# Optimization experiments

Measured on AMD Instinct MI355X. Metric: run time of the kernel, lower is better.

The kernel has to match this reference:

```python
import jax, jax.numpy as jnp
import numpy as np

N_HEAD = 16
N_KV_HEAD = 4
D_MODEL = 2048
D_HEAD = 128
D_OUT = 2048
N_REP = N_HEAD // N_KV_HEAD
Q_INNER = N_HEAD * D_HEAD
KV_INNER = N_KV_HEAD * D_HEAD
B, S = 2, 2048


def setup_inputs() -> dict:
    key = jax.random.key(0)
    ks = jax.random.split(key, 10)
    sc = lambda fan_in: 1.0 / np.sqrt(fan_in)
    return {
        "hidden_state": jax.random.normal(ks[0], (B, S, D_MODEL), dtype=jnp.float32),
        "attention_mask": jnp.ones((B, 1, S, S), dtype=jnp.int32),
        "Wq": jax.random.uniform(ks[1], (Q_INNER, D_MODEL), jnp.float32, -sc(D_MODEL), sc(D_MODEL)),
        "bq": jax.random.uniform(ks[2], (Q_INNER,), jnp.float32, -sc(D_MODEL), sc(D_MODEL)),
        "Wk": jax.random.uniform(ks[3], (KV_INNER, D_MODEL), jnp.float32, -sc(D_MODEL), sc(D_MODEL)),
        "bk": jax.random.uniform(ks[4], (KV_INNER,), jnp.float32, -sc(D_MODEL), sc(D_MODEL)),
        "Wv": jax.random.uniform(ks[5], (KV_INNER, D_MODEL), jnp.float32, -sc(D_MODEL), sc(D_MODEL)),
        "bv": jax.random.uniform(ks[6], (KV_INNER,), jnp.float32, -sc(D_MODEL), sc(D_MODEL)),
        "Wo": jax.random.uniform(ks[7], (D_OUT, Q_INNER), jnp.float32, -sc(Q_INNER), sc(Q_INNER)),
        "bo": jax.random.uniform(ks[8], (D_OUT,), jnp.float32, -sc(Q_INNER), sc(Q_INNER)),
    }


def reference(hidden_state, attention_mask, Wq, bq, Wk, bk, Wv, bv, Wo, bo):
    b, s, _ = hidden_state.shape
    # projections (torch Linear: x @ W.T + b)
    q = hidden_state @ Wq.T + bq                    # [b, s, n_head*d_head]
    k = hidden_state @ Wk.T + bk                    # [b, s, n_kv*d_head]
    v = hidden_state @ Wv.T + bv
    q = q.reshape(b, s, N_HEAD, D_HEAD).transpose(0, 2, 1, 3)      # [b, h, s, d]
    k = k.reshape(b, s, N_KV_HEAD, D_HEAD).transpose(0, 2, 1, 3)   # [b, kh, s, d]
    v = v.reshape(b, s, N_KV_HEAD, D_HEAD).transpose(0, 2, 1, 3)
    # repeat_kv: expand kv heads to n_head
    k = jnp.repeat(k, N_REP, axis=1)                # [b, h, s, d]
    v = jnp.repeat(v, N_REP, axis=1)
    scores = jnp.einsum("bhqd,bhkd->bhqk", q, k) / jnp.sqrt(jnp.float32(D_HEAD))
    scores = jnp.where(attention_mask == 0, -jnp.inf, scores)
    probs = jax.nn.softmax(scores, axis=-1)         # [b, h, s, s]
    out = jnp.einsum("bhqk,bhkd->bhqd", probs, v)   # [b, h, s, d]
    out = out.transpose(0, 2, 1, 3).reshape(b, s, Q_INNER)
    return out @ Wo.T + bo                          # [b, s, d_out]
```

## Files before the change

### kernel.cpp

```cpp
#include <hip/hip_runtime.h>

typedef unsigned short u16;
typedef unsigned int u32;
typedef __attribute__((ext_vector_type(4))) float f32x4;
typedef __attribute__((ext_vector_type(16))) float f32x16;
typedef __attribute__((ext_vector_type(2))) u32 u32x2;
typedef __attribute__((ext_vector_type(4))) u32 u32x4;
typedef __attribute__((ext_vector_type(8))) __bf16 bf16x8;

#define QSCALE (0.08838834764831845f * 1.44269504088896340736f)

__device__ __forceinline__ u16 f2bf(float x) {
  u32 u = __builtin_bit_cast(u32, x);
  u32 r = (u + 0x7FFFu + ((u >> 16) & 1u)) >> 16;
  return (u16)r;
}

__device__ __forceinline__ u16 cvt_bf16(float x) {
  __bf16 b = (__bf16)x;
  return __builtin_bit_cast(u16, b);
}

__device__ __forceinline__ u32 pk2(float lo, float hi) {
  return (u32)cvt_bf16(lo) | ((u32)cvt_bf16(hi) << 16);
}

__device__ __forceinline__ f32x16 mfma32(bf16x8 a, bf16x8 b, f32x16 c) {
  return __builtin_amdgcn_mfma_f32_32x32x16_bf16(a, b, c, 0, 0, 0);
}

#define GLDS16(g, l)                                              \
  __builtin_amdgcn_global_load_lds(                               \
      (const __attribute__((address_space(1))) void*)(g),         \
      (__attribute__((address_space(3))) void*)(l), 16, 0, 0)

__global__ __launch_bounds__(256) void cvt_kernel(const float* __restrict__ src,
                                                  u16* __restrict__ dst) {
  size_t i = (size_t)blockIdx.x * 256 + threadIdx.x;
  float4 a = ((const float4*)src)[2 * i];
  float4 b = ((const float4*)src)[2 * i + 1];
  uint4 r;
  r.x = f2bf(a.x) | ((u32)f2bf(a.y) << 16);
  r.y = f2bf(a.z) | ((u32)f2bf(a.w) << 16);
  r.z = f2bf(b.x) | ((u32)f2bf(b.y) << 16);
  r.w = f2bf(b.z) | ((u32)f2bf(b.w) << 16);
  ((uint4*)dst)[i] = r;
}

__device__ __forceinline__ void gemm_bt_core(const u16* __restrict__ A,
                                             const u16* __restrict__ B, int K,
                                             int bm, int bn, u16* As, u16* Bs,
                                             f32x4 acc[4][4]) {
  const int tid = threadIdx.x;
  const int lane = tid & 63;
  const int w = tid >> 6;
  const int wm = (w >> 1) * 64;
  const int wn = (w & 1) * 64;
  const int r0 = lane & 15;
  const int g = lane >> 4;
  const int c = w * 64 + lane;
  const int arow = c >> 2;
  const int acol = (c & 3) * 8;

  for (int k0 = 0; k0 < K; k0 += 32) {
    GLDS16(A + (size_t)(bm + arow) * K + k0 + acol, As + w * 512);
    GLDS16(A + (size_t)(bm + 64 + arow) * K + k0 + acol, As + 2048 + w * 512);
    GLDS16(B + (size_t)(bn + arow) * K + k0 + acol, Bs + w * 512);
    GLDS16(B + (size_t)(bn + 64 + arow) * K + k0 + acol, Bs + 2048 + w * 512);
    __syncthreads();
    bf16x8 af[4], bf[4];
#pragma unroll
    for (int mi = 0; mi < 4; ++mi)
      af[mi] = *(const bf16x8*)&As[(wm + mi * 16 + r0) * 32 + g * 8];
#pragma unroll
    for (int ni = 0; ni < 4; ++ni)
      bf[ni] = *(const bf16x8*)&Bs[(wn + ni * 16 + r0) * 32 + g * 8];
#pragma unroll
    for (int mi = 0; mi < 4; ++mi)
#pragma unroll
      for (int ni = 0; ni < 4; ++ni)
        acc[mi][ni] = __builtin_amdgcn_mfma_f32_16x16x32_bf16(af[mi], bf[ni],
                                                              acc[mi][ni], 0, 0, 0);
    __syncthreads();
  }
}

__global__ __launch_bounds__(256, 2) void qkv_gemm(
    const u16* __restrict__ A, const u16* __restrict__ B,
    const float* __restrict__ bq, const float* __restrict__ bk,
    const float* __restrict__ bv, u16* __restrict__ qb, u16* __restrict__ kb,
    u16* __restrict__ vtb) {
  __shared__ u16 As[4096], Bs[4096];
  f32x4 acc[4][4];
#pragma unroll
  for (int i = 0; i < 4; ++i)
#pragma unroll
    for (int j = 0; j < 4; ++j) acc[i][j] = f32x4{0.f, 0.f, 0.f, 0.f};
  const int bm = blockIdx.y * 128, bn = blockIdx.x * 128;
  gemm_bt_core(A, B, 2048, bm, bn, As, Bs, acc);
  const int lane = threadIdx.x & 63, w = threadIdx.x >> 6;
  const int wm = (w >> 1) * 64, wn = (w & 1) * 64;
  const int r0 = lane & 15, g = lane >> 4;
#pragma unroll
  for (int ni = 0; ni < 4; ++ni) {
    const int n = bn + wn + ni * 16 + r0;
#pragma unroll
    for (int mi = 0; mi < 4; ++mi) {
      f32x4 v = acc[mi][ni];
#pragma unroll
      for (int r = 0; r < 4; ++r) {
        const int m = bm + wm + mi * 16 + g * 4 + r;
        const int b = m >> 11, s = m & 2047;
        const float val = v[r];
        if (n < 2048) {
          const int h = n >> 7, d = n & 127;
          qb[((size_t)(b * 16 + h) * 2048 + s) * 128 + d] =
              f2bf((val + bq[n]) * QSCALE);
        } else if (n < 2560) {
          const int nn = n - 2048, kh = nn >> 7, d = nn & 127;
          kb[((size_t)(b * 4 + kh) * 2048 + s) * 128 + d] = f2bf(val + bk[nn]);
        } else {
          const int nn = n - 2560, kh = nn >> 7, d = nn & 127;
          vtb[((size_t)(b * 4 + kh) * 128 + d) * 2048 + s] = f2bf(val + bv[nn]);
        }
      }
    }
  }
}

__global__ __launch_bounds__(256, 2) void oproj_gemm(const u16* __restrict__ A,
                                                     const u16* __restrict__ B,
                                                     const float* __restrict__ bo,
                                                     float* __restrict__ out) {
  __shared__ u16 As[4096], Bs[4096];
  f32x4 acc[4][4];
#pragma unroll
  for (int i = 0; i < 4; ++i)
#pragma unroll
    for (int j = 0; j < 4; ++j) acc[i][j] = f32x4{0.f, 0.f, 0.f, 0.f};
  const int bm = blockIdx.y * 128, bn = blockIdx.x * 128;
  gemm_bt_core(A, B, 2048, bm, bn, As, Bs, acc);
  const int lane = threadIdx.x & 63, w = threadIdx.x >> 6;
  const int wm = (w >> 1) * 64, wn = (w & 1) * 64;
  const int r0 = lane & 15, g = lane >> 4;
#pragma unroll
  for (int ni = 0; ni < 4; ++ni) {
    const int n = bn + wn + ni * 16 + r0;
    const float bb = bo[n];
#pragma unroll
    for (int mi = 0; mi < 4; ++mi) {
#pragma unroll
      for (int r = 0; r < 4; ++r) {
        const int m = bm + wm + mi * 16 + g * 4 + r;
        out[(size_t)m * 2048 + n] = acc[mi][ni][r] + bb;
      }
    }
  }
}

__global__ __launch_bounds__(256, 2) void attn_kernel(const u16* __restrict__ q,
                                                      const u16* __restrict__ k,
                                                      const u16* __restrict__ vt,
                                                      u16* __restrict__ o) {
  __shared__ u16 Ks[2][8192];
  __shared__ u16 Vs[2][8192];
  const int tid = threadIdx.x, lane = tid & 63, w = tid >> 6;
  const int l31 = lane & 31, hi = lane >> 5;
  const int b = blockIdx.z, h = blockIdx.y, kh = h >> 2;
  const int q0 = blockIdx.x * 128 + w * 32;
  const u16* qh = q + ((size_t)(b * 16 + h) * 2048 + q0) * 128;
  const u16* kp = k + (size_t)(b * 4 + kh) * 2048 * 128;
  const u16* vp = vt + (size_t)(b * 4 + kh) * 128 * 2048;

  bf16x8 qa[8];
#pragma unroll
  for (int dc = 0; dc < 8; ++dc)
    qa[dc] = *(const bf16x8*)&qh[(size_t)l31 * 128 + dc * 16 + hi * 8];

  f32x16 oacc[4];
#pragma unroll
  for (int dt = 0; dt < 4; ++dt) oacc[dt] = (f32x16)(0.f);
  float mrun = -INFINITY, lrun = 0.f;

  const int gB = w * 64 + lane;

#define STAGE_KV(cur, t)                                                       \
  do {                                                                         \
    const u16* kt_ = kp + (size_t)(t) * 64 * 128;                              \
    _Pragma("unroll") for (int i_ = 0; i_ < 4; ++i_) {                         \
      int gi_ = i_ * 256 + gB;                                                 \
      int row_ = gi_ >> 4, gc_ = gi_ & 15;                                     \
      GLDS16(kt_ + row_ * 128 + ((gc_ ^ (row_ & 15)) * 8),                     \
             &Ks[cur][(i_ * 256 + w * 64) * 8]);                               \
    }                                                                          \
    _Pragma("unroll") for (int i_ = 0; i_ < 4; ++i_) {                         \
      int gi_ = i_ * 256 + gB;                                                 \
      int row_ = gi_ >> 3, gc_ = gi_ & 7;                                      \
      GLDS16(vp + (size_t)row_ * 2048 + (t) * 64 + ((gc_ ^ (row_ & 7)) * 8),   \
             &Vs[cur][(i_ * 256 + w * 64) * 8]);                               \
    }                                                                          \
  } while (0)

  STAGE_KV(0, 0);
  __syncthreads();
  int cur = 0;

  for (int t = 0; t < 32; ++t) {
    if (t < 31) STAGE_KV(cur ^ 1, t + 1);

    f32x16 s0v = (f32x16)(0.f), s1v = (f32x16)(0.f);
    __builtin_amdgcn_s_setprio(1);
#pragma unroll
    for (int dc = 0; dc < 8; ++dc) {
      const int gc = dc * 2 + hi;
      const int ro0 = l31, ro1 = 32 + l31;
      bf16x8 kf0 = *(const bf16x8*)&Ks[cur][ro0 * 128 + ((gc ^ (ro0 & 15)) << 3)];
      bf16x8 kf1 = *(const bf16x8*)&Ks[cur][ro1 * 128 + ((gc ^ (ro1 & 15)) << 3)];
      s0v = mfma32(kf0, qa[dc], s0v);
      s1v = mfma32(kf1, qa[dc], s1v);
    }
    __builtin_amdgcn_s_setprio(0);

    float m8[8];
#pragma unroll
    for (int i = 0; i < 8; ++i)
      m8[i] = fmaxf(fmaxf(s0v[i], s0v[i + 8]), fmaxf(s1v[i], s1v[i + 8]));
    float mx = fmaxf(fmaxf(fmaxf(m8[0], m8[1]), fmaxf(m8[2], m8[3])),
                     fmaxf(fmaxf(m8[4], m8[5]), fmaxf(m8[6], m8[7])));
    mx = fmaxf(mx, __shfl_xor(mx, 32));
    if (__any(mx > mrun + 8.f)) {
      const float mnew = fmaxf(mrun, mx);
      const float alpha = __builtin_amdgcn_exp2f(mrun - mnew);
      mrun = mnew;
      lrun *= alpha;
#pragma unroll
      for (int r = 0; r < 16; ++r) {
        const float ar = __shfl(alpha, ((r & 3) + 8 * (r >> 2)) + (hi << 2));
#pragma unroll
        for (int dt = 0; dt < 4; ++dt) oacc[dt][r] *= ar;
      }
    }
    float rsf = 0.f;
#pragma unroll
    for (int i = 0; i < 16; ++i) {
      s0v[i] = __builtin_amdgcn_exp2f(s0v[i] - mrun);
      s1v[i] = __builtin_amdgcn_exp2f(s1v[i] - mrun);
      rsf += s0v[i] + s1v[i];
    }
    lrun += rsf + __shfl_xor(rsf, 32);

    __builtin_amdgcn_s_setprio(1);
#pragma unroll
    for (int c = 0; c < 4; ++c) {
      const float* sv = (c < 2) ? (const float*)&s0v : (const float*)&s1v;
      const int base = (c & 1) * 8;
      u32x4 fw;
      fw[0] = pk2(sv[base + 0], sv[base + 1]);
      fw[1] = pk2(sv[base + 2], sv[base + 3]);
      fw[2] = pk2(sv[base + 4], sv[base + 5]);
      fw[3] = pk2(sv[base + 6], sv[base + 7]);
      const bf16x8 pf = __builtin_bit_cast(bf16x8, fw);
#pragma unroll
      for (int dt = 0; dt < 4; ++dt) {
        const int d = dt * 32 + l31;
        const u32x2 vlo =
            *(const u32x2*)&Vs[cur][d * 64 + (((2 * c) ^ (d & 7)) << 3) + 4 * hi];
        const u32x2 vhi =
            *(const u32x2*)&Vs[cur][d * 64 + (((2 * c + 1) ^ (d & 7)) << 3) + 4 * hi];
        u32x4 vv;
        vv[0] = vlo[0]; vv[1] = vlo[1]; vv[2] = vhi[0]; vv[3] = vhi[1];
        oacc[dt] = mfma32(pf, __builtin_bit_cast(bf16x8, vv), oacc[dt]);
      }
    }
    __builtin_amdgcn_s_setprio(0);

    __syncthreads();
    cur ^= 1;
  }
#undef STAGE_KV

  const float invl = 1.f / lrun;
#pragma unroll
  for (int r = 0; r < 16; ++r) {
    const int rb = (r & 3) + 8 * (r >> 2);
    const float linv = __shfl(invl, rb + (hi << 2));
    const int row = q0 + rb + (hi << 2);
#pragma unroll
    for (int dt = 0; dt < 4; ++dt)
      o[(size_t)(b * 2048 + row) * 2048 + h * 128 + dt * 32 + l31] =
          cvt_bf16(oacc[dt][r] * linv);
  }
}

extern "C" void kernel_launch(void* const* d_in, const int* in_sizes, int n_in,
                              void* d_out, int out_size, void* d_ws,
                              size_t ws_size, hipStream_t stream) {
  (void)in_sizes; (void)n_in; (void)out_size; (void)ws_size;
  const float* hidden = (const float*)d_in[0];
  const float* Wq = (const float*)d_in[2];
  const float* bq = (const float*)d_in[3];
  const float* Wk = (const float*)d_in[4];
  const float* bk = (const float*)d_in[5];
  const float* Wv = (const float*)d_in[6];
  const float* bv = (const float*)d_in[7];
  const float* Wo = (const float*)d_in[8];
  const float* bo = (const float*)d_in[9];
  float* out = (float*)d_out;
  char* ws = (char*)d_ws;

  u16* hidb = (u16*)(ws + 0);
  u16* wcat = (u16*)(ws + 16777216);
  u16* wob  = (u16*)(ws + 29360128);
  u16* qb   = (u16*)(ws + 37748736);
  u16* kb   = (u16*)(ws + 54525952);
  u16* vtb  = (u16*)(ws + 58720256);
  u16* attb = (u16*)(ws + 62914560);

  cvt_kernel<<<4096, 256, 0, stream>>>(hidden, hidb);
  cvt_kernel<<<2048, 256, 0, stream>>>(Wq, wcat);
  cvt_kernel<<<512, 256, 0, stream>>>(Wk, wcat + (size_t)2048 * 2048);
  cvt_kernel<<<512, 256, 0, stream>>>(Wv, wcat + (size_t)2560 * 2048);
  cvt_kernel<<<2048, 256, 0, stream>>>(Wo, wob);

  qkv_gemm<<<dim3(24, 32), 256, 0, stream>>>(hidb, wcat, bq, bk, bv, qb, kb, vtb);
  attn_kernel<<<dim3(16, 16, 2), 256, 0, stream>>>(qb, kb, vtb, attb);
  oproj_gemm<<<dim3(16, 32), 256, 0, stream>>>(attb, wob, bo, out);
}
```

Before: 231.0 us.

## Merge conversion launches, widen GEMM K-tile with swizzle, compute softmax denominator via MFMA

Fuses the five fp32-to-bf16 conversion launches into one kernel that picks its source and destination by block index, removing per-launch overhead. The shared GEMM core now stages 64-wide K slices with an XOR-swizzled LDS layout. This halves the barriers per K step and avoids LDS bank conflicts, at the cost of doubling LDS per block. In attention, the row-sum of probabilities is computed by an extra MFMA against a ones vector instead of scalar adds and shuffles, trading VALU work for matrix-core work.

```diff
diff --git a/kernel.cpp b/kernel.cpp
--- a/kernel.cpp
+++ b/kernel.cpp
@@ -34,17 +34,29 @@
       (const __attribute__((address_space(1))) void*)(g),         \
       (__attribute__((address_space(3))) void*)(l), 16, 0, 0)
 
-__global__ __launch_bounds__(256) void cvt_kernel(const float* __restrict__ src,
-                                                  u16* __restrict__ dst) {
-  size_t i = (size_t)blockIdx.x * 256 + threadIdx.x;
-  float4 a = ((const float4*)src)[2 * i];
-  float4 b = ((const float4*)src)[2 * i + 1];
+__global__ __launch_bounds__(256) void cvt5_kernel(
+    const float* __restrict__ s0, const float* __restrict__ s1,
+    const float* __restrict__ s2, const float* __restrict__ s3,
+    const float* __restrict__ s4, u16* __restrict__ d0, u16* __restrict__ d1,
+    u16* __restrict__ d2, u16* __restrict__ d3, u16* __restrict__ d4) {
+  const int bid = blockIdx.x;
+  const float* s;
+  u16* d;
+  int base;
+  if (bid < 4096) { s = s0; d = d0; base = 0; }
+  else if (bid < 6144) { s = s1; d = d1; base = 4096; }
+  else if (bid < 6656) { s = s2; d = d2; base = 6144; }
+  else if (bid < 7168) { s = s3; d = d3; base = 6656; }
+  else { s = s4; d = d4; base = 7168; }
+  size_t i = (size_t)(bid - base) * 256 + threadIdx.x;
+  float4 a = ((const float4*)s)[2 * i];
+  float4 b = ((const float4*)s)[2 * i + 1];
   uint4 r;
   r.x = f2bf(a.x) | ((u32)f2bf(a.y) << 16);
   r.y = f2bf(a.z) | ((u32)f2bf(a.w) << 16);
   r.z = f2bf(b.x) | ((u32)f2bf(b.y) << 16);
   r.w = f2bf(b.z) | ((u32)f2bf(b.w) << 16);
-  ((uint4*)dst)[i] = r;
+  ((uint4*)d)[i] = r;
 }
 
 __device__ __forceinline__ void gemm_bt_core(const u16* __restrict__ A,
@@ -58,29 +70,37 @@
   const int wn = (w & 1) * 64;
   const int r0 = lane & 15;
   const int g = lane >> 4;
-  const int c = w * 64 + lane;
-  const int arow = c >> 2;
-  const int acol = (c & 3) * 8;
-
-  for (int k0 = 0; k0 < K; k0 += 32) {
-    GLDS16(A + (size_t)(bm + arow) * K + k0 + acol, As + w * 512);
-    GLDS16(A + (size_t)(bm + 64 + arow) * K + k0 + acol, As + 2048 + w * 512);
-    GLDS16(B + (size_t)(bn + arow) * K + k0 + acol, Bs + w * 512);
-    GLDS16(B + (size_t)(bn + 64 + arow) * K + k0 + acol, Bs + 2048 + w * 512);
+
+  for (int k0 = 0; k0 < K; k0 += 64) {
+#pragma unroll
+    for (int i = 0; i < 4; ++i) {
+      const int gi = i * 256 + tid;
+      const int row = gi >> 3, gc = gi & 7;
+      const int scol = (gc ^ (row & 7)) * 8;
+      GLDS16(A + (size_t)(bm + row) * K + k0 + scol, As + gi * 8);
+      GLDS16(B + (size_t)(bn + row) * K + k0 + scol, Bs + gi * 8);
+    }
     __syncthreads();
-    bf16x8 af[4], bf[4];
-#pragma unroll
-    for (int mi = 0; mi < 4; ++mi)
-      af[mi] = *(const bf16x8*)&As[(wm + mi * 16 + r0) * 32 + g * 8];
-#pragma unroll
-    for (int ni = 0; ni < 4; ++ni)
-      bf[ni] = *(const bf16x8*)&Bs[(wn + ni * 16 + r0) * 32 + g * 8];
-#pragma unroll
-    for (int mi = 0; mi < 4; ++mi)
-#pragma unroll
-      for (int ni = 0; ni < 4; ++ni)
-        acc[mi][ni] = __builtin_amdgcn_mfma_f32_16x16x32_bf16(af[mi], bf[ni],
-                                                              acc[mi][ni], 0, 0, 0);
+#pragma unroll
+    for (int kh = 0; kh < 2; ++kh) {
+      bf16x8 af[4], bf[4];
+#pragma unroll
+      for (int mi = 0; mi < 4; ++mi) {
+        const int row = wm + mi * 16 + r0;
+        af[mi] = *(const bf16x8*)&As[row * 64 + (((kh * 4 + g) ^ (row & 7)) * 8)];
+      }
+#pragma unroll
+      for (int ni = 0; ni < 4; ++ni) {
+        const int row = wn + ni * 16 + r0;
+        bf[ni] = *(const bf16x8*)&Bs[row * 64 + (((kh * 4 + g) ^ (row & 7)) * 8)];
+      }
+#pragma unroll
+      for (int mi = 0; mi < 4; ++mi)
+#pragma unroll
+        for (int ni = 0; ni < 4; ++ni)
+          acc[mi][ni] = __builtin_amdgcn_mfma_f32_16x16x32_bf16(
+              af[mi], bf[ni], acc[mi][ni], 0, 0, 0);
+    }
     __syncthreads();
   }
 }
@@ -90,7 +110,7 @@
     const float* __restrict__ bq, const float* __restrict__ bk,
     const float* __restrict__ bv, u16* __restrict__ qb, u16* __restrict__ kb,
     u16* __restrict__ vtb) {
-  __shared__ u16 As[4096], Bs[4096];
+  __shared__ u16 As[8192], Bs[8192];
   f32x4 acc[4][4];
 #pragma unroll
   for (int i = 0; i < 4; ++i)
@@ -132,7 +152,7 @@
                                                      const u16* __restrict__ B,
                                                      const float* __restrict__ bo,
                                                      float* __restrict__ out) {
-  __shared__ u16 As[4096], Bs[4096];
+  __shared__ u16 As[8192], Bs[8192];
   f32x4 acc[4][4];
 #pragma unroll
   for (int i = 0; i < 4; ++i)
@@ -180,7 +200,12 @@
   f32x16 oacc[4];
 #pragma unroll
   for (int dt = 0; dt < 4; ++dt) oacc[dt] = (f32x16)(0.f);
-  float mrun = -INFINITY, lrun = 0.f;
+  f32x16 lacc = (f32x16)(0.f);
+  float mrun = -INFINITY;
+
+  u32x4 onev;
+  onev[0] = onev[1] = onev[2] = onev[3] = 0x3F803F80u;
+  const bf16x8 ones_b = __builtin_bit_cast(bf16x8, onev);
 
   const int gB = w * 64 + lane;
 
@@ -232,22 +257,19 @@
       const float mnew = fmaxf(mrun, mx);
       const float alpha = __builtin_amdgcn_exp2f(mrun - mnew);
       mrun = mnew;
-      lrun *= alpha;
 #pragma unroll
       for (int r = 0; r < 16; ++r) {
         const float ar = __shfl(alpha, ((r & 3) + 8 * (r >> 2)) + (hi << 2));
+        lacc[r] *= ar;
 #pragma unroll
         for (int dt = 0; dt < 4; ++dt) oacc[dt][r] *= ar;
       }
     }
-    float rsf = 0.f;
 #pragma unroll
     for (int i = 0; i < 16; ++i) {
       s0v[i] = __builtin_amdgcn_exp2f(s0v[i] - mrun);
       s1v[i] = __builtin_amdgcn_exp2f(s1v[i] - mrun);
-      rsf += s0v[i] + s1v[i];
-    }
-    lrun += rsf + __shfl_xor(rsf, 32);
+    }
 
     __builtin_amdgcn_s_setprio(1);
 #pragma unroll
@@ -260,6 +282,7 @@
       fw[2] = pk2(sv[base + 4], sv[base + 5]);
       fw[3] = pk2(sv[base + 6], sv[base + 7]);
       const bf16x8 pf = __builtin_bit_cast(bf16x8, fw);
+      lacc = mfma32(pf, ones_b, lacc);
 #pragma unroll
       for (int dt = 0; dt < 4; ++dt) {
         const int d = dt * 32 + l31;
@@ -279,12 +302,10 @@
   }
 #undef STAGE_KV
 
-  const float invl = 1.f / lrun;
 #pragma unroll
   for (int r = 0; r < 16; ++r) {
-    const int rb = (r & 3) + 8 * (r >> 2);
-    const float linv = __shfl(invl, rb + (hi << 2));
-    const int row = q0 + rb + (hi << 2);
+    const float linv = 1.f / lacc[r];
+    const int row = q0 + (r & 3) + 8 * (r >> 2) + (hi << 2);
 #pragma unroll
     for (int dt = 0; dt < 4; ++dt)
       o[(size_t)(b * 2048 + row) * 2048 + h * 128 + dt * 32 + l31] =
@@ -316,11 +337,9 @@
   u16* vtb  = (u16*)(ws + 58720256);
   u16* attb = (u16*)(ws + 62914560);
 
-  cvt_kernel<<<4096, 256, 0, stream>>>(hidden, hidb);
-  cvt_kernel<<<2048, 256, 0, stream>>>(Wq, wcat);
-  cvt_kernel<<<512, 256, 0, stream>>>(Wk, wcat + (size_t)2048 * 2048);
-  cvt_kernel<<<512, 256, 0, stream>>>(Wv, wcat + (size_t)2560 * 2048);
-  cvt_kernel<<<2048, 256, 0, stream>>>(Wo, wob);
+  cvt5_kernel<<<9216, 256, 0, stream>>>(hidden, Wq, Wk, Wv, Wo, hidb, wcat,
+                                        wcat + (size_t)2048 * 2048,
+                                        wcat + (size_t)2560 * 2048, wob);
 
   qkv_gemm<<<dim3(24, 32), 256, 0, stream>>>(hidb, wcat, bq, bk, bv, qb, kb, vtb);
   attn_kernel<<<dim3(16, 16, 2), 256, 0, stream>>>(qb, kb, vtb, attb);
```

New measurement: 209.6 us. 9.2% less time.
